# Kernel optimization log

Hardware: AMD Instinct MI355X
Metric: run time of the kernel (lower is better)

The kernel has to match this reference:

```python
import jax, jax.numpy as jnp
import numpy as np

EPS = 1e-6
H = 8  # num_heads

def _ln(x, gamma, beta):
    mu = jnp.mean(x, axis=-1, keepdims=True)
    var = jnp.mean(jnp.square(x - mu), axis=-1, keepdims=True)
    return (x - mu) * jax.lax.rsqrt(var + EPS) * gamma + beta

def setup_inputs() -> dict:
    key = jax.random.key(0)
    ks = jax.random.split(key, 10)
    b, n_sink, n_src = 2, 1024, 4096
    sink_dim, src_dim, hid = 512, 512, 512
    s = 0.02
    return {
        "sink": jax.random.normal(ks[0], (b, n_sink, sink_dim), jnp.float32),
        "source": jax.random.normal(ks[1], (b, n_src, src_dim), jnp.float32),
        "gamma_s": jnp.ones((sink_dim,), jnp.float32),
        "beta_s": jnp.zeros((sink_dim,), jnp.float32),
        "gamma_c": jnp.ones((src_dim,), jnp.float32),
        "beta_c": jnp.zeros((src_dim,), jnp.float32),
        "Wq": jax.random.normal(ks[2], (sink_dim, hid), jnp.float32) * s,
        "bq": jnp.zeros((hid,), jnp.float32),
        "Wkv": jax.random.normal(ks[3], (src_dim, 2 * hid), jnp.float32) * s,
        "bkv": jnp.zeros((2 * hid,), jnp.float32),
        "Wo": jax.random.normal(ks[4], (hid, sink_dim), jnp.float32) * s,
        "bo": jnp.zeros((sink_dim,), jnp.float32),
    }

def reference(sink, source, gamma_s, beta_s, gamma_c, beta_c, Wq, bq, Wkv, bkv, Wo, bo):
    b, n_sink, _ = sink.shape
    n_src = source.shape[1]
    hid = Wq.shape[1]
    d = hid // H
    scale = d ** -0.5
    # pre-norm
    s = _ln(sink, gamma_s, beta_s)
    c = _ln(source, gamma_c, beta_c)
    # projections -> [b, h, n, d]
    q = (s @ Wq + bq).reshape(b, n_sink, H, d).transpose(0, 2, 1, 3)
    kv = c @ Wkv + bkv
    k, v = jnp.split(kv, 2, axis=-1)
    k = k.reshape(b, n_src, H, d).transpose(0, 2, 1, 3)
    v = v.reshape(b, n_src, H, d).transpose(0, 2, 1, 3)
    sim = jnp.einsum('bhid,bhjd->bhij', q, k) * scale  # [b,h,i,j]
    # sink competition: softmax over query axis i, then renormalize over keys j
    attn = jax.nn.softmax(sim, axis=-2) + EPS
    attn = attn / jnp.sum(attn, axis=-1, keepdims=True)
    out = jnp.einsum('bhij,bhjd->bhid', attn, v)
    out = out.transpose(0, 2, 1, 3).reshape(b, n_sink, hid)
    return out @ Wo + bo
```

## Files before the change

### kernel.cpp

```cpp
#include <hip/hip_runtime.h>
#include <hip/hip_bf16.h>
#include <math.h>

#define EPS 1e-6f
#define NSINK 1024
#define NSRC 4096
#define DIM 512
#define NH 8
#define HD 64
#define BATCH 2
#define QSCALE 0.18033688011112042f

#if __has_builtin(__builtin_amdgcn_permlane32_swap) && __has_builtin(__builtin_amdgcn_permlane16_swap)
#define HAVE_PERMLANE 1
#else
#define HAVE_PERMLANE 0
#endif

typedef unsigned short u16;
typedef __attribute__((ext_vector_type(8))) short short8;
typedef __attribute__((ext_vector_type(4))) float f32x4;

__device__ inline float fast_exp2(float x) {
#if __has_builtin(__builtin_amdgcn_exp2f)
    return __builtin_amdgcn_exp2f(x);
#else
    return exp2f(x);
#endif
}
__device__ inline float fast_rcp(float x) {
#if __has_builtin(__builtin_amdgcn_rcpf)
    return __builtin_amdgcn_rcpf(x);
#else
    return 1.0f / x;
#endif
}
__device__ inline u16 f2bf(float x) {
    union { float f; unsigned u; } v; v.f = x;
    unsigned r = v.u + 0x7fffu + ((v.u >> 16) & 1u);
    return (u16)(r >> 16);
}
__device__ inline float bf2f(u16 h) {
    union { unsigned u; float f; } v; v.u = ((unsigned)h) << 16;
    return v.f;
}
__device__ inline unsigned pk_bf16(float a, float b) {
    union { __hip_bfloat162 h; unsigned u; } v;
    v.h = __float22bfloat162_rn(make_float2(a, b));
    return v.u;
}
__device__ inline f32x4 mfma16(short8 a, short8 b, f32x4 c) {
    return __builtin_amdgcn_mfma_f32_16x16x32_bf16(a, b, c, 0, 0, 0);
}
__device__ inline short8 ldfrag(const u16* base, int stride, int lane) {
    return *(const short8*)(base + (size_t)(lane & 15) * stride + ((lane >> 4) << 3));
}

__device__ inline void gld16(const u16* g, u16* l) {
    __builtin_amdgcn_global_load_lds(
        (const __attribute__((address_space(1))) unsigned*)g,
        (__attribute__((address_space(3))) unsigned*)l, 16, 0, 0);
}

template<int TM>
__device__ inline void stage_tile(u16* lds, const u16* gsrc, int K, int t) {
    #pragma unroll
    for (int it = 0; it < TM / 32; ++it) {
        int m = it * 32 + (t >> 3);
        int c = (t & 7) ^ (m & 7);
        gld16(gsrc + (size_t)m * K + c * 8,
              lds + it * 2048 + (t >> 6) * 512);
    }
}
__device__ inline short8 rdfrag(const u16* tile, int fbase, int cbase, int lane) {
    int m = fbase + (lane & 15);
    int c = (cbase + (lane >> 4)) ^ (m & 7);
    return *(const short8*)(tile + (size_t)m * 64 + c * 8);
}

#if HAVE_PERMLANE
__device__ inline short8 pa_frag(const f32x4 sA, const f32x4 sB) {
    unsigned A0 = pk_bf16(sA[0], sA[1]);
    unsigned A1 = pk_bf16(sA[2], sA[3]);
    unsigned B0 = pk_bf16(sB[0], sB[1]);
    unsigned B1 = pk_bf16(sB[2], sB[3]);
    auto c0 = __builtin_amdgcn_permlane32_swap(A0, B0, false, false);
    auto c1 = __builtin_amdgcn_permlane32_swap(A1, B1, false, false);
    auto d0 = __builtin_amdgcn_permlane16_swap(c0[0], c0[1], false, false);
    auto d1 = __builtin_amdgcn_permlane16_swap(c1[0], c1[1], false, false);
    union { unsigned u[4]; short8 s8; } r;
    r.u[0] = d0[0]; r.u[1] = d1[0]; r.u[2] = d0[1]; r.u[3] = d1[1];
    return r.s8;
}
#endif

__global__ __launch_bounds__(256) void prep(
    const float* __restrict__ sink, const float* __restrict__ source,
    const float* __restrict__ gs, const float* __restrict__ bs,
    const float* __restrict__ gc, const float* __restrict__ bc,
    const float* __restrict__ Wq, const float* __restrict__ Wkv,
    const float* __restrict__ Wo,
    u16* __restrict__ sh, u16* __restrict__ ch,
    u16* __restrict__ wqT, u16* __restrict__ wkvT, u16* __restrict__ woT)
{
    int row = blockIdx.x;
    int t = threadIdx.x;
    if (row >= BATCH * (NSINK + NSRC)) {
        int n = row - BATCH * (NSINK + NSRC);
        const float* W; u16* T; int N; int nn;
        if (n < 512)       { W = Wq;  T = wqT;  N = 512;  nn = n; }
        else if (n < 1536) { W = Wkv; T = wkvT; N = 1024; nn = n - 512; }
        else               { W = Wo;  T = woT;  N = 512;  nn = n - 1536; }
        for (int k = t; k < 512; k += 256)
            T[(size_t)nn * 512 + k] = f2bf(W[(size_t)k * N + nn]);
        return;
    }
    const float* xr; const float* g; const float* be; u16* y;
    if (row < BATCH * NSINK) {
        xr = sink + (size_t)row * DIM; g = gs; be = bs; y = sh + (size_t)row * DIM;
    } else {
        int rr = row - BATCH * NSINK;
        xr = source + (size_t)rr * DIM; g = gc; be = bc; y = ch + (size_t)rr * DIM;
    }
    float v0 = xr[t], v1 = xr[t + 256];
    float s = v0 + v1, sq = v0 * v0 + v1 * v1;
    #pragma unroll
    for (int off = 32; off > 0; off >>= 1) {
        s  += __shfl_down(s, off, 64);
        sq += __shfl_down(sq, off, 64);
    }
    __shared__ float rsm[4], rq[4];
    int wave = t >> 6;
    if ((t & 63) == 0) { rsm[wave] = s; rq[wave] = sq; }
    __syncthreads();
    s  = rsm[0] + rsm[1] + rsm[2] + rsm[3];
    sq = rq[0] + rq[1] + rq[2] + rq[3];
    float mu = s * (1.0f / DIM);
    float var = sq * (1.0f / DIM) - mu * mu;
    float a = var + EPS;
    float r = rsqrtf(a);
    r = r * (1.5f - 0.5f * a * r * r);
    y[t]       = f2bf((v0 - mu) * r * g[t] + be[t]);
    y[t + 256] = f2bf((v1 - mu) * r * g[t + 256] + be[t + 256]);
}

template<int MODE, int TM, int TN, int SWZ>
__global__ __launch_bounds__(256) void gemm1(
    const u16* __restrict__ A, const u16* __restrict__ BT,
    const float* __restrict__ bias, int K,
    float* __restrict__ cf, u16* __restrict__ o1, u16* __restrict__ o2)
{
    constexpr int FM = TM / 32, FN = TN / 32;
    __shared__ u16 As[2][TM * 64];
    __shared__ u16 Bs[2][TN * 64];
    int t = threadIdx.x;
    int wave = t >> 6, lane = t & 63;
    int wr = wave >> 1, wc = wave & 1;
    int m0, n0;
    if constexpr (SWZ) {
        int id = blockIdx.x;
        int slot = id >> 3;
        m0 = ((id & 7) * 8 + (slot & 7)) * TM;
        n0 = (slot >> 3) * TN;
    } else {
        m0 = blockIdx.y * TM;
        n0 = blockIdx.x * TN;
    }

    f32x4 acc[FM][FN] = {};
    stage_tile<TM>(As[0], A + (size_t)m0 * K, K, t);
    stage_tile<TN>(Bs[0], BT + (size_t)n0 * K, K, t);
    __syncthreads();
    int nt = K >> 6;
    int cur = 0;
    for (int kt = 0; kt < nt; ++kt) {
        if (kt + 1 < nt) {
            stage_tile<TM>(As[cur ^ 1], A + (size_t)m0 * K + (kt + 1) * 64, K, t);
            stage_tile<TN>(Bs[cur ^ 1], BT + (size_t)n0 * K + (kt + 1) * 64, K, t);
        }
        #pragma unroll
        for (int kk = 0; kk < 2; ++kk) {
            short8 af[FM], bf[FN];
            #pragma unroll
            for (int f = 0; f < FM; ++f)
                af[f] = rdfrag(As[cur], wr * (TM / 2) + f * 16, kk * 4, lane);
            #pragma unroll
            for (int f = 0; f < FN; ++f)
                bf[f] = rdfrag(Bs[cur], wc * (TN / 2) + f * 16, kk * 4, lane);
            #pragma unroll
            for (int i = 0; i < FM; ++i)
                #pragma unroll
                for (int j = 0; j < FN; ++j)
                    acc[i][j] = mfma16(af[i], bf[j], acc[i][j]);
        }
        __syncthreads();
        cur ^= 1;
    }

    #pragma unroll
    for (int i = 0; i < FM; ++i)
        #pragma unroll
        for (int j = 0; j < FN; ++j)
            #pragma unroll
            for (int r = 0; r < 4; ++r) {
                int m = m0 + wr * (TM / 2) + i * 16 + (lane >> 4) * 4 + r;
                int n = n0 + wc * (TN / 2) + j * 16 + (lane & 15);
                float v = acc[i][j][r] + bias[n];
                if (MODE == 0) {
                    cf[(size_t)m * DIM + n] = v;
                } else if (MODE == 1) {
                    int b = m >> 10, ii = m & 1023;
                    int h = n >> 6, d = n & 63;
                    o1[((size_t)(b * NH + h) * NSINK + ii) * HD + d] = f2bf(v * QSCALE);
                } else {
                    int b = m >> 12, jj = m & 4095;
                    if (n < DIM) {
                        int h = n >> 6, d = n & 63;
                        o1[((size_t)(b * NH + h) * NSRC + jj) * HD + d] = f2bf(v);
                    } else {
                        int nn = n - DIM;
                        int h = nn >> 6, d = nn & 63;
                        o2[((size_t)(b * NH + h) * HD + d) * NSRC + jj] = f2bf(v);
                    }
                }
            }
}

__global__ __launch_bounds__(256, 4) void pass_a(const u16* __restrict__ q,
    const u16* __restrict__ k, float* __restrict__ part)
{
    int id = blockIdx.x;
    int slot = id >> 3;
    int bh = (id & 7) + 8 * (slot >> 6);
    int rem = slot & 63;
    int ic = rem >> 4;
    int t = threadIdx.x, wave = t >> 6, lane = t & 63;
    int j0 = (rem & 15) * 256 + wave * 64;
    const u16* qb = q + (size_t)bh * NSINK * HD;
    const u16* kb = k + (size_t)bh * NSRC * HD;

    __shared__ u16 Qs[2][64 * 64];

    short8 kf[4][2];
    #pragma unroll
    for (int jf = 0; jf < 4; ++jf)
        #pragma unroll
        for (int kc = 0; kc < 2; ++kc)
            kf[jf][kc] = ldfrag(kb + (size_t)(j0 + jf * 16) * HD + kc * 32, HD, lane);

    float csum[4] = {};
    stage_tile<64>(Qs[0], qb + (size_t)(ic * 256) * HD, HD, t);
    __syncthreads();
    int cur = 0;
    for (int ii = 0; ii < 4; ++ii) {
        if (ii + 1 < 4)
            stage_tile<64>(Qs[cur ^ 1], qb + (size_t)(ic * 256 + (ii + 1) * 64) * HD, HD, t);
        #pragma unroll
        for (int f = 0; f < 4; ++f) {
            short8 q0 = rdfrag(Qs[cur], f * 16, 0, lane);
            short8 q1 = rdfrag(Qs[cur], f * 16, 4, lane);
            f32x4 s[4] = {};
            #pragma unroll
            for (int jf = 0; jf < 4; ++jf) s[jf] = mfma16(q0, kf[jf][0], s[jf]);
            #pragma unroll
            for (int jf = 0; jf < 4; ++jf) s[jf] = mfma16(q1, kf[jf][1], s[jf]);
            #pragma unroll
            for (int jf = 0; jf < 4; ++jf)
                csum[jf] += fast_exp2(s[jf][0]) + fast_exp2(s[jf][1])
                          + fast_exp2(s[jf][2]) + fast_exp2(s[jf][3]);
        }
        __syncthreads();
        cur ^= 1;
    }
    #pragma unroll
    for (int jf = 0; jf < 4; ++jf) {
        csum[jf] += __shfl_xor(csum[jf], 16, 64);
        csum[jf] += __shfl_xor(csum[jf], 32, 64);
    }
    if (lane < 16)
        #pragma unroll
        for (int jf = 0; jf < 4; ++jf)
            part[((size_t)ic * BATCH * NH + bh) * NSRC + j0 + jf * 16 + lane] = csum[jf];
}

__global__ __launch_bounds__(256) void csred_vsum(const float* __restrict__ part,
    const u16* __restrict__ vTh, float* __restrict__ rcs, float* __restrict__ vs)
{
    int blk = blockIdx.x;
    if (blk < 256) {
        int x = blk * 256 + threadIdx.x;
        const int S = BATCH * NH * NSRC;
        float cs = part[x] + part[x + S] + part[x + 2 * S] + part[x + 3 * S];
        rcs[x] = fast_rcp(cs);
        return;
    }
    int row = blk - 256;
    const u16* ph = vTh + (size_t)row * NSRC;
    float s = 0.f;
    for (int j = threadIdx.x; j < NSRC; j += 256) s += bf2f(ph[j]);
    #pragma unroll
    for (int off = 32; off > 0; off >>= 1) s += __shfl_down(s, off, 64);
    __shared__ float r4[4];
    if ((threadIdx.x & 63) == 0) r4[threadIdx.x >> 6] = s;
    __syncthreads();
    if (threadIdx.x == 0) vs[row] = r4[0] + r4[1] + r4[2] + r4[3];
}

__global__ __launch_bounds__(256, 3) void pass_b(const u16* __restrict__ q,
    const u16* __restrict__ k, const u16* __restrict__ vTh,
    const float* __restrict__ rcs, u16* __restrict__ pvb, float* __restrict__ rs)
{
    int id = blockIdx.x;
    int slot = id >> 3;
    int bh = (id & 7) + 8 * (slot >> 5);
    int rem = slot & 31;
    int split = rem >> 3;
    int i0 = (rem & 7) * 128;
    int t = threadIdx.x, wave = t >> 6, lane = t & 63;
    const u16* qb = q + (size_t)bh * NSINK * HD;
    const u16* kb = k + (size_t)bh * NSRC * HD;
    const u16* vb = vTh + (size_t)bh * HD * NSRC;
    const float* rc = rcs + (size_t)bh * NSRC;

    __shared__ u16 Ks[2][64 * 64];
    __shared__ u16 Vs[2][64 * 64];
    __shared__ alignas(16) float RcsF[2][64];
#if !HAVE_PERMLANE
    __shared__ alignas(16) u16 pbuf[4][2][16 * 76];
#endif

    short8 qf[2][2];
    #pragma unroll
    for (int fi = 0; fi < 2; ++fi)
        #pragma unroll
        for (int kc = 0; kc < 2; ++kc)
            qf[fi][kc] = ldfrag(qb + (size_t)(i0 + wave * 32 + fi * 16) * HD + kc * 32, HD, lane);

    short8 ones8;
    #pragma unroll
    for (int i = 0; i < 8; ++i) ones8[i] = (short)0x3F80;
    short8 z = {};
    short8 b5 = ((lane & 15) == 0) ? ones8 : z;

    auto stage = [&](int buf, int jt) {
        int j0 = split * (NSRC / 4) + jt * 64;
        stage_tile<64>(Ks[buf], kb + (size_t)j0 * HD, HD, t);
        stage_tile<64>(Vs[buf], vb + j0, NSRC, t);
        if (t < 16) gld16((const u16*)(rc + j0) + t * 8, (u16*)RcsF[buf]);
    };

    f32x4 o[2][5] = {};
    stage(0, 0);
    __syncthreads();
    int cur = 0;
    for (int jt = 0; jt < 16; ++jt) {
        if (jt + 1 < 16) stage(cur ^ 1, jt + 1);
        f32x4 s[2][4] = {};
        #pragma unroll
        for (int kc = 0; kc < 2; ++kc)
            #pragma unroll
            for (int jf = 0; jf < 4; ++jf) {
                short8 kf = rdfrag(Ks[cur], jf * 16, kc * 4, lane);
                s[0][jf] = mfma16(kf, qf[0][kc], s[0][jf]);
                s[1][jf] = mfma16(kf, qf[1][kc], s[1][jf]);
            }
        #pragma unroll
        for (int jf = 0; jf < 4; ++jf) {
            f32x4 rcv = *(const f32x4*)&RcsF[cur][jf * 16 + ((lane >> 4) << 2)];
            #pragma unroll
            for (int fi = 0; fi < 2; ++fi)
                #pragma unroll
                for (int r = 0; r < 4; ++r)
                    s[fi][jf][r] = fast_exp2(s[fi][jf][r]) * rcv[r];
        }
#if !HAVE_PERMLANE
        #pragma unroll
        for (int fi = 0; fi < 2; ++fi)
            #pragma unroll
            for (int jf = 0; jf < 4; ++jf) {
                uint2 w;
                w.x = pk_bf16(s[fi][jf][0], s[fi][jf][1]);
                w.y = pk_bf16(s[fi][jf][2], s[fi][jf][3]);
                *(uint2*)&pbuf[wave][fi][(size_t)(lane & 15) * 76 + jf * 16 + (lane >> 4) * 4] = w;
            }
#endif
        #pragma unroll
        for (int jc = 0; jc < 2; ++jc) {
#if HAVE_PERMLANE
            short8 pa0 = pa_frag(s[0][2 * jc], s[0][2 * jc + 1]);
            short8 pa1 = pa_frag(s[1][2 * jc], s[1][2 * jc + 1]);
#else
            short8 pa0 = *(const short8*)&pbuf[wave][0][(size_t)(lane & 15) * 76 + jc * 32 + (lane >> 4) * 8];
            short8 pa1 = *(const short8*)&pbuf[wave][1][(size_t)(lane & 15) * 76 + jc * 32 + (lane >> 4) * 8];
#endif
            #pragma unroll
            for (int df = 0; df < 4; ++df) {
                short8 vf = rdfrag(Vs[cur], df * 16, jc * 4, lane);
                o[0][df] = mfma16(pa0, vf, o[0][df]);
                o[1][df] = mfma16(pa1, vf, o[1][df]);
            }
            o[0][4] = mfma16(pa0, b5, o[0][4]);
            o[1][4] = mfma16(pa1, b5, o[1][4]);
        }
        __syncthreads();
        cur ^= 1;
    }
    if ((lane & 15) == 0) {
        #pragma unroll
        for (int fi = 0; fi < 2; ++fi)
            #pragma unroll
            for (int r = 0; r < 4; ++r)
                rs[((size_t)split * (BATCH * NH) + bh) * NSINK + i0 + wave * 32 + fi * 16 + (lane >> 4) * 4 + r] = o[fi][4][r];
    }
    int b = bh >> 3, h = bh & 7;
    u16* pvp = pvb + (size_t)split * BATCH * NSINK * DIM;
    #pragma unroll
    for (int fi = 0; fi < 2; ++fi)
        #pragma unroll
        for (int df = 0; df < 4; ++df)
            #pragma unroll
            for (int r = 0; r < 4; ++r) {
                int row = i0 + wave * 32 + fi * 16 + (lane >> 4) * 4 + r;
                pvp[((size_t)(b * NSINK + row)) * DIM + h * HD + df * 16 + (lane & 15)] = f2bf(o[fi][df][r]);
            }
}

__global__ __launch_bounds__(256) void finalize_pv(const u16* __restrict__ pvb,
    const float* __restrict__ rs, const float* __restrict__ vs,
    u16* __restrict__ ab)
{
    const int M = BATCH * NSINK * DIM;
    const int R = BATCH * NH * NSINK;
    int idx = blockIdx.x * 256 + threadIdx.x;
    int m = idx >> 9, n = idx & 511;
    int b = m >> 10, i = m & 1023, h = n >> 6, d = n & 63;
    int bh = b * NH + h;
    float val = bf2f(pvb[idx]) + bf2f(pvb[idx + M]) + bf2f(pvb[idx + 2 * M])
              + bf2f(pvb[idx + 3 * M]) + EPS * vs[bh * HD + d];
    float rsv = rs[bh * NSINK + i] + rs[R + bh * NSINK + i]
              + rs[2 * R + bh * NSINK + i] + rs[3 * R + bh * NSINK + i]
              + (float)NSRC * EPS;
    ab[idx] = f2bf(val / rsv);
}

extern "C" void kernel_launch(void* const* d_in, const int* in_sizes, int n_in,
                              void* d_out, int out_size, void* d_ws, size_t ws_size,
                              hipStream_t stream) {
    (void)in_sizes; (void)n_in; (void)out_size;
    const float* sink    = (const float*)d_in[0];
    const float* source  = (const float*)d_in[1];
    const float* gamma_s = (const float*)d_in[2];
    const float* beta_s  = (const float*)d_in[3];
    const float* gamma_c = (const float*)d_in[4];
    const float* beta_c  = (const float*)d_in[5];
    const float* Wq      = (const float*)d_in[6];
    const float* bq      = (const float*)d_in[7];
    const float* Wkv     = (const float*)d_in[8];
    const float* bkv     = (const float*)d_in[9];
    const float* Wo      = (const float*)d_in[10];
    const float* bo      = (const float*)d_in[11];
    float* out = (float*)d_out;

    char* p = (char*)d_ws;
    auto carve = [&](size_t bytes) { char* r = p; p += (bytes + 255) & ~(size_t)255; return r; };
    u16* sh    = (u16*)carve(2048ull * 512 * 2);
    u16* ch    = (u16*)carve(8192ull * 512 * 2);
    u16* wqT   = (u16*)carve(512ull * 512 * 2);
    u16* wkvT  = (u16*)carve(1024ull * 512 * 2);
    u16* woT   = (u16*)carve(512ull * 512 * 2);
    u16* qb    = (u16*)carve(16ull * 1024 * 64 * 2);
    u16* kb    = (u16*)carve(16ull * 4096 * 64 * 2);
    u16* vTh   = (u16*)carve(16ull * 64 * 4096 * 2);
    float* cs_part = (float*)carve(4ull * 16 * 4096 * 4);
    float* rcs     = (float*)carve(16ull * 4096 * 4);
    float* vs      = (float*)carve(1024ull * 4);
    float* rs      = (float*)carve(4ull * 16 * 1024 * 4);
    u16*   pvb     = (u16*)carve(4ull * 2048 * 512 * 2);
    u16*   ab      = (u16*)carve(2048ull * 512 * 2);
    if ((size_t)(p - (char*)d_ws) > ws_size) return;

    prep<<<BATCH * (NSINK + NSRC) + 2048, 256, 0, stream>>>(
        sink, source, gamma_s, beta_s, gamma_c, beta_c,
        Wq, Wkv, Wo, sh, ch, wqT, wkvT, woT);

    gemm1<1, 64, 64, 0><<<dim3(DIM / 64, BATCH * NSINK / 64), 256, 0, stream>>>(
        sh, wqT, bq, 512, nullptr, qb, nullptr);
    gemm1<2, 128, 128, 1><<<512, 256, 0, stream>>>(
        ch, wkvT, bkv, 512, nullptr, kb, vTh);

    pass_a<<<1024, 256, 0, stream>>>(qb, kb, cs_part);
    csred_vsum<<<256 + 1024, 256, 0, stream>>>(cs_part, vTh, rcs, vs);
    pass_b<<<512, 256, 0, stream>>>(qb, kb, vTh, rcs, pvb, rs);
    finalize_pv<<<4096, 256, 0, stream>>>(pvb, rs, vs, ab);

    gemm1<0, 64, 64, 0><<<dim3(DIM / 64, BATCH * NSINK / 64), 256, 0, stream>>>(
        ab, woT, bo, 512, out, nullptr, nullptr);
}
```

Baseline: 106.6 us.

## Merge Q and KV projection GEMMs into one launch; stage V transpose through LDS

The separate Q-projection and KV-projection GEMM launches become one kernel that picks its sub-problem from the block index. This removes a launch and lets the small Q GEMM run alongside the KV GEMM. The V half of the KV projection now writes its transposed output through a shared-memory buffer, so each thread stores contiguous 8-byte chunks along the sequence axis instead of scattered 2-byte writes. The fused kernel reserves 64KB of LDS for every block, which may lower occupancy for the small Q tiles.

```diff
diff --git a/kernel.cpp b/kernel.cpp
--- a/kernel.cpp
+++ b/kernel.cpp
@@ -144,49 +144,38 @@
     y[t + 256] = f2bf((v1 - mu) * r * g[t + 256] + be[t + 256]);
 }
 
-template<int MODE, int TM, int TN, int SWZ>
-__global__ __launch_bounds__(256) void gemm1(
+template<int MODE, int TM, int TN>
+__device__ inline void gemm_body(u16* smem, int m0, int n0,
     const u16* __restrict__ A, const u16* __restrict__ BT,
     const float* __restrict__ bias, int K,
-    float* __restrict__ cf, u16* __restrict__ o1, u16* __restrict__ o2)
+    float* __restrict__ cf, u16* __restrict__ o1, u16* __restrict__ o2, int t)
 {
     constexpr int FM = TM / 32, FN = TN / 32;
-    __shared__ u16 As[2][TM * 64];
-    __shared__ u16 Bs[2][TN * 64];
-    int t = threadIdx.x;
+    u16* Asb[2] = { smem, smem + TM * 64 };
+    u16* Bsb[2] = { smem + 2 * TM * 64, smem + 2 * TM * 64 + TN * 64 };
     int wave = t >> 6, lane = t & 63;
     int wr = wave >> 1, wc = wave & 1;
-    int m0, n0;
-    if constexpr (SWZ) {
-        int id = blockIdx.x;
-        int slot = id >> 3;
-        m0 = ((id & 7) * 8 + (slot & 7)) * TM;
-        n0 = (slot >> 3) * TN;
-    } else {
-        m0 = blockIdx.y * TM;
-        n0 = blockIdx.x * TN;
-    }
 
     f32x4 acc[FM][FN] = {};
-    stage_tile<TM>(As[0], A + (size_t)m0 * K, K, t);
-    stage_tile<TN>(Bs[0], BT + (size_t)n0 * K, K, t);
+    stage_tile<TM>(Asb[0], A + (size_t)m0 * K, K, t);
+    stage_tile<TN>(Bsb[0], BT + (size_t)n0 * K, K, t);
     __syncthreads();
     int nt = K >> 6;
     int cur = 0;
     for (int kt = 0; kt < nt; ++kt) {
         if (kt + 1 < nt) {
-            stage_tile<TM>(As[cur ^ 1], A + (size_t)m0 * K + (kt + 1) * 64, K, t);
-            stage_tile<TN>(Bs[cur ^ 1], BT + (size_t)n0 * K + (kt + 1) * 64, K, t);
+            stage_tile<TM>(Asb[cur ^ 1], A + (size_t)m0 * K + (kt + 1) * 64, K, t);
+            stage_tile<TN>(Bsb[cur ^ 1], BT + (size_t)n0 * K + (kt + 1) * 64, K, t);
         }
         #pragma unroll
         for (int kk = 0; kk < 2; ++kk) {
             short8 af[FM], bf[FN];
             #pragma unroll
             for (int f = 0; f < FM; ++f)
-                af[f] = rdfrag(As[cur], wr * (TM / 2) + f * 16, kk * 4, lane);
+                af[f] = rdfrag(Asb[cur], wr * (TM / 2) + f * 16, kk * 4, lane);
             #pragma unroll
             for (int f = 0; f < FN; ++f)
-                bf[f] = rdfrag(Bs[cur], wc * (TN / 2) + f * 16, kk * 4, lane);
+                bf[f] = rdfrag(Bsb[cur], wc * (TN / 2) + f * 16, kk * 4, lane);
             #pragma unroll
             for (int i = 0; i < FM; ++i)
                 #pragma unroll
@@ -195,6 +184,33 @@
         }
         __syncthreads();
         cur ^= 1;
+    }
+
+    if (MODE == 2 && n0 >= DIM) {
+        u16* tb = smem;
+        #pragma unroll
+        for (int i = 0; i < FM; ++i)
+            #pragma unroll
+            for (int j = 0; j < FN; ++j) {
+                int nl = wc * (TN / 2) + j * 16 + (lane & 15);
+                int ml = wr * (TM / 2) + i * 16 + ((lane >> 4) << 2);
+                float bia = bias[n0 + nl];
+                union { u16 h[4]; uint2 v; } pk;
+                #pragma unroll
+                for (int r = 0; r < 4; ++r) pk.h[r] = f2bf(acc[i][j][r] + bia);
+                *(uint2*)&tb[(size_t)nl * 140 + ml] = pk.v;
+            }
+        __syncthreads();
+        int rowl = t >> 1, seg = t & 1;
+        int nn = n0 + rowl - DIM;
+        int h = nn >> 6, d = nn & 63;
+        int b = m0 >> 12, jj0 = m0 & 4095;
+        u16* dst = o2 + ((size_t)(b * NH + h) * HD + d) * NSRC + jj0 + seg * 64;
+        const u16* sp = tb + (size_t)rowl * 140 + seg * 64;
+        #pragma unroll
+        for (int c = 0; c < 16; ++c)
+            *(uint2*)(dst + c * 4) = *(const uint2*)(sp + c * 4);
+        return;
     }
 
     #pragma unroll
@@ -214,16 +230,40 @@
                     o1[((size_t)(b * NH + h) * NSINK + ii) * HD + d] = f2bf(v * QSCALE);
                 } else {
                     int b = m >> 12, jj = m & 4095;
-                    if (n < DIM) {
-                        int h = n >> 6, d = n & 63;
-                        o1[((size_t)(b * NH + h) * NSRC + jj) * HD + d] = f2bf(v);
-                    } else {
-                        int nn = n - DIM;
-                        int h = nn >> 6, d = nn & 63;
-                        o2[((size_t)(b * NH + h) * HD + d) * NSRC + jj] = f2bf(v);
-                    }
+                    int h = n >> 6, d = n & 63;
+                    o1[((size_t)(b * NH + h) * NSRC + jj) * HD + d] = f2bf(v);
                 }
             }
+}
+
+__global__ __launch_bounds__(256) void gemm_qkv(
+    const u16* __restrict__ sh, const u16* __restrict__ ch,
+    const u16* __restrict__ wqT, const u16* __restrict__ wkvT,
+    const float* __restrict__ bq, const float* __restrict__ bkv,
+    u16* __restrict__ qb, u16* __restrict__ kb, u16* __restrict__ vTh)
+{
+    __shared__ u16 smem[32768];
+    int id = blockIdx.x, t = threadIdx.x;
+    if (id < 512) {
+        int slot = id >> 3;
+        int m0 = ((id & 7) * 8 + (slot & 7)) * 128;
+        int n0 = (slot >> 3) * 128;
+        gemm_body<2, 128, 128>(smem, m0, n0, ch, wkvT, bkv, 512, nullptr, kb, vTh, t);
+    } else {
+        int q = id - 512;
+        int m0 = (q >> 3) * 64;
+        int n0 = (q & 7) * 64;
+        gemm_body<1, 64, 64>(smem, m0, n0, sh, wqT, bq, 512, nullptr, qb, nullptr, t);
+    }
+}
+
+__global__ __launch_bounds__(256) void gemm_o(
+    const u16* __restrict__ ab, const u16* __restrict__ woT,
+    const float* __restrict__ bo, float* __restrict__ out)
+{
+    __shared__ u16 smem[16384];
+    gemm_body<0, 64, 64>(smem, blockIdx.y * 64, blockIdx.x * 64,
+                         ab, woT, bo, 512, out, nullptr, nullptr, threadIdx.x);
 }
 
 __global__ __launch_bounds__(256, 4) void pass_a(const u16* __restrict__ q,
@@ -483,16 +523,12 @@
         sink, source, gamma_s, beta_s, gamma_c, beta_c,
         Wq, Wkv, Wo, sh, ch, wqT, wkvT, woT);
 
-    gemm1<1, 64, 64, 0><<<dim3(DIM / 64, BATCH * NSINK / 64), 256, 0, stream>>>(
-        sh, wqT, bq, 512, nullptr, qb, nullptr);
-    gemm1<2, 128, 128, 1><<<512, 256, 0, stream>>>(
-        ch, wkvT, bkv, 512, nullptr, kb, vTh);
+    gemm_qkv<<<768, 256, 0, stream>>>(sh, ch, wqT, wkvT, bq, bkv, qb, kb, vTh);
 
     pass_a<<<1024, 256, 0, stream>>>(qb, kb, cs_part);
     csred_vsum<<<256 + 1024, 256, 0, stream>>>(cs_part, vTh, rcs, vs);
     pass_b<<<512, 256, 0, stream>>>(qb, kb, vTh, rcs, pvb, rs);
     finalize_pv<<<4096, 256, 0, stream>>>(pvb, rs, vs, ab);
 
-    gemm1<0, 64, 64, 0><<<dim3(DIM / 64, BATCH * NSINK / 64), 256, 0, stream>>>(
-        ab, woT, bo, 512, out, nullptr, nullptr);
-}
+    gemm_o<<<dim3(DIM / 64, BATCH * NSINK / 64), 256, 0, stream>>>(ab, woT, bo, out);
+}
```

After: 98.49 us, median of 2. 1.08x faster.
